# Kernel optimization log

Measured on AMD Instinct MI355X. Metric: run time of the kernel, lower is better.

The kernel has to match this reference:

```python
import jax, jax.numpy as jnp
import numpy as np


def setup_inputs() -> dict:
    key = jax.random.key(0)
    k1, k2, k3 = jax.random.split(key, 3)
    N, M, D, K = 8192, 8192, 512, 128
    x = jax.random.normal(k1, (N, D), dtype=jnp.float32)
    target = jax.random.normal(k2, (M, D), dtype=jnp.float32)
    W = jax.random.normal(k3, (D, K), dtype=jnp.float32) * 0.05
    return {"x": x, "target": target, "W": W}


def reference(x, target, W):
    # phi_Brenier(x): convex potential f(x) = logsumexp(x @ W)  -> [N]
    phi_b = jax.nn.logsumexp(x @ W, axis=-1)
    # phi_Kantorovich = 0.5||x||^2 - phi_Brenier  -> [N]
    x_sq = jnp.sum(x * x, axis=-1)
    phi_k = 0.5 * x_sq - phi_b
    t_sq = jnp.sum(target * target, axis=-1)
    DD = 0.5 * (x_sq[:, None] + t_sq[None, :] - 2.0 * (x @ target.T))
    # C-transform: min over source points  -> [M]
    phi_c = jnp.min(DD - phi_k[:, None], axis=0)
    # Kantorovich dual objective (scalar)
    return jnp.mean(phi_k) + jnp.mean(phi_c)
```

## Files before the change

### kernel.cpp

```cpp
#include <hip/hip_runtime.h>
#include <hip/hip_bf16.h>
#include <stdint.h>

typedef __attribute__((ext_vector_type(8))) short short8;
typedef __attribute__((ext_vector_type(4))) float f32x4;
typedef __attribute__((ext_vector_type(16))) float f32x16;
typedef __attribute__((ext_vector_type(4))) int i32x4;
typedef __attribute__((ext_vector_type(8))) int i32x8;

#define N_PTS 8192
#define M_PTS 8192
#define DIM   512
#define KDIM  128

__device__ __forceinline__ unsigned fenc(float f) {
  unsigned u = __float_as_uint(f);
  return (u & 0x80000000u) ? ~u : (u | 0x80000000u);
}
__device__ __forceinline__ float fdec(unsigned k) {
  unsigned u = (k & 0x80000000u) ? (k ^ 0x80000000u) : ~k;
  return __uint_as_float(u);
}

__device__ __forceinline__ unsigned short f2bf(float f) {
  union { __hip_bfloat16 h; unsigned short u; } c;
  c.h = __float2bfloat16(f);
  return c.u;
}

__device__ __forceinline__ unsigned f2e4m3(float f) {
  unsigned u = __float_as_uint(f);
  unsigned s = (u >> 24) & 0x80;
  unsigned mag = u & 0x7fffffffu;
  unsigned r = mag + 0x0007ffffu + ((mag >> 20) & 1u);
  int e = (int)(r >> 23) - 127;
  if (e < -6) return s;
  unsigned m = (r >> 20) & 7u;
  return s | (unsigned)((e + 7) << 3) | m;
}

__device__ __forceinline__ void async_copy16(const void* g, void* l) {
  __builtin_amdgcn_global_load_lds(
      (const __attribute__((address_space(1))) void*)g,
      (__attribute__((address_space(3))) void*)l, 16, 0, 0);
}

__device__ __forceinline__ int swz_slot(int row, int slot) {
  return slot ^ ((row >> 1) & 3);
}

__device__ __forceinline__ int chunk_key(int row) {
  return ((row >> 1) & 3) ^ ((row >> 3) & 1) ^ (((row >> 4) & 1) << 1);
}

#define BARRIER __builtin_amdgcn_s_barrier()

__global__ __launch_bounds__(256)
void prep_all_kernel(const float* __restrict__ x, const float* __restrict__ tgt,
                     const float* __restrict__ W,
                     unsigned short* __restrict__ Xb, unsigned char* __restrict__ Xf8,
                     unsigned char* __restrict__ TfT, unsigned short* __restrict__ WbT,
                     float* __restrict__ xsq, float* __restrict__ tsq,
                     unsigned* __restrict__ keys) {
  const int bid = blockIdx.x;
  const int tid = threadIdx.x;
  if (bid >= (N_PTS + M_PTS) / 4) {
    const int o = (bid - (N_PTS + M_PTS) / 4) * 256 + tid;
    const int k = o >> 9, d = o & 511;
    WbT[o] = f2bf(W[d * KDIM + k]);
    return;
  }
  const int gw = (bid * 256 + tid) >> 6;
  const int j = tid & 63;
  float s;
  if (gw < N_PTS) {
    const float* src = x + (size_t)gw * DIM + j * 8;
    float4 v0 = *(const float4*)src;
    float4 v1 = *(const float4*)(src + 4);
    s = v0.x * v0.x + v0.y * v0.y + v0.z * v0.z + v0.w * v0.w +
        v1.x * v1.x + v1.y * v1.y + v1.z * v1.z + v1.w * v1.w;
    unsigned short* db = Xb + (size_t)gw * DIM + j * 8;
    ushort4 ob0, ob1;
    ob0.x = f2bf(v0.x); ob0.y = f2bf(v0.y); ob0.z = f2bf(v0.z); ob0.w = f2bf(v0.w);
    ob1.x = f2bf(v1.x); ob1.y = f2bf(v1.y); ob1.z = f2bf(v1.z); ob1.w = f2bf(v1.w);
    *(ushort4*)db = ob0;
    *(ushort4*)(db + 4) = ob1;
    unsigned long long p = (unsigned long long)f2e4m3(v0.x)
        | ((unsigned long long)f2e4m3(v0.y) << 8)
        | ((unsigned long long)f2e4m3(v0.z) << 16)
        | ((unsigned long long)f2e4m3(v0.w) << 24)
        | ((unsigned long long)f2e4m3(v1.x) << 32)
        | ((unsigned long long)f2e4m3(v1.y) << 40)
        | ((unsigned long long)f2e4m3(v1.z) << 48)
        | ((unsigned long long)f2e4m3(v1.w) << 56);
    *(unsigned long long*)(Xf8 + (size_t)gw * DIM + j * 8) = p;
#pragma unroll
    for (int m = 1; m <= 32; m <<= 1) s += __shfl_xor(s, m);
    if (j == 0) xsq[gw] = s;
  } else {
    const int tr = gw - N_PTS;
    const float* src = tgt + (size_t)tr * DIM + j * 8;
    float4 v0 = *(const float4*)src;
    float4 v1 = *(const float4*)(src + 4);
    s = v0.x * v0.x + v0.y * v0.y + v0.z * v0.z + v0.w * v0.w +
        v1.x * v1.x + v1.y * v1.y + v1.z * v1.z + v1.w * v1.w;
    unsigned long long p = (unsigned long long)f2e4m3(v0.x)
        | ((unsigned long long)f2e4m3(v0.y) << 8)
        | ((unsigned long long)f2e4m3(v0.z) << 16)
        | ((unsigned long long)f2e4m3(v0.w) << 24)
        | ((unsigned long long)f2e4m3(v1.x) << 32)
        | ((unsigned long long)f2e4m3(v1.y) << 40)
        | ((unsigned long long)f2e4m3(v1.z) << 48)
        | ((unsigned long long)f2e4m3(v1.w) << 56);
    *(unsigned long long*)(TfT + ((size_t)(j >> 3) * M_PTS + tr) * 64 + (j & 7) * 8) = p;
#pragma unroll
    for (int m = 1; m <= 32; m <<= 1) s += __shfl_xor(s, m);
    if (j == 0) { tsq[tr] = s; keys[tr] = 0xFFFFFFFFu; }
  }
}

__global__ __launch_bounds__(256)
void phi_b_kernel(const short* __restrict__ Xb, const short* __restrict__ WbT,
                  float* __restrict__ phi_b) {
  __shared__ __align__(16) short As[32 * 32];
  __shared__ __align__(16) short Bs[128 * 32];
  __shared__ __align__(16) float lg[32][136];

  const int tid = threadIdx.x;
  const int wave = tid >> 6, lane = tid & 63;
  const int n0 = blockIdx.x * 32;
  const int fr = lane & 15, g = lane >> 4;
  const int wc = wave;

  const int srow = tid >> 2;
  const int sk8 = swz_slot(srow, tid & 3) * 8;
  const int ra = tid >> 2;
  const int ska = swz_slot(ra, tid & 3) * 8;

  f32x4 acc[2][2] = {};
  for (int kt = 0; kt < 16; ++kt) {
    const int k0 = kt * 32;
    if (wave < 2)
      async_copy16(Xb + (size_t)(n0 + ra) * DIM + k0 + ska, &As[wave * 512]);
    async_copy16(WbT + (size_t)srow * DIM + k0 + sk8, &Bs[wave * 512]);
    async_copy16(WbT + (size_t)(srow + 64) * DIM + k0 + sk8, &Bs[2048 + wave * 512]);
    __syncthreads();
    short8 a[2], b[2];
#pragma unroll
    for (int i = 0; i < 2; ++i) {
      const int R = i * 16 + fr;
      a[i] = *(const short8*)&As[R * 32 + swz_slot(R, g) * 8];
    }
#pragma unroll
    for (int jx = 0; jx < 2; ++jx) {
      const int R = wc * 32 + jx * 16 + fr;
      b[jx] = *(const short8*)&Bs[R * 32 + swz_slot(R, g) * 8];
    }
#pragma unroll
    for (int i = 0; i < 2; ++i)
#pragma unroll
      for (int jx = 0; jx < 2; ++jx)
        acc[i][jx] = __builtin_amdgcn_mfma_f32_16x16x32_bf16(a[i], b[jx], acc[i][jx], 0, 0, 0);
    __syncthreads();
  }

  const int rq = g * 4;
#pragma unroll
  for (int i = 0; i < 2; ++i)
#pragma unroll
    for (int jx = 0; jx < 2; ++jx)
#pragma unroll
      for (int q = 0; q < 4; ++q)
        lg[i * 16 + rq + q][wc * 32 + jx * 16 + fr] = acc[i][jx][q];
  __syncthreads();

  const int row = tid >> 3, c8 = tid & 7;
  const float4* lr = (const float4*)(&lg[row][c8 * 16]);
  float mx = -3.4e38f;
#pragma unroll
  for (int c = 0; c < 4; ++c) {
    float4 v = lr[c];
    mx = fmaxf(mx, fmaxf(fmaxf(v.x, v.y), fmaxf(v.z, v.w)));
  }
  mx = fmaxf(mx, __shfl_xor(mx, 1));
  mx = fmaxf(mx, __shfl_xor(mx, 2));
  mx = fmaxf(mx, __shfl_xor(mx, 4));
  float s = 0.f;
#pragma unroll
  for (int c = 0; c < 4; ++c) {
    float4 v = lr[c];
    s += __expf(v.x - mx) + __expf(v.y - mx) + __expf(v.z - mx) + __expf(v.w - mx);
  }
  s += __shfl_xor(s, 1);
  s += __shfl_xor(s, 2);
  s += __shfl_xor(s, 4);
  if (c8 == 0) phi_b[n0 + row] = mx + logf(s);
}

__device__ __forceinline__ void stgA(const unsigned char* __restrict__ mat,
                                     int rowbase, int kbyte,
                                     unsigned char* dst, int tid) {
  const int r = tid >> 2, d = tid & 3;
  async_copy16(mat + (size_t)(rowbase + r) * DIM + kbyte + ((d ^ chunk_key(r)) << 4),
               dst + (tid >> 6) * 1024);
}

__device__ __forceinline__ i32x8 ld2x16(const unsigned char* p0, const unsigned char* p1) {
  i32x4 lo = *(const i32x4*)p0;
  i32x4 hi = *(const i32x4*)p1;
  return __builtin_shufflevector(lo, hi, 0, 1, 2, 3, 4, 5, 6, 7);
}

__device__ __forceinline__ f32x16 mfma_mx(i32x8 a, i32x8 b, f32x16 c) {
  return __builtin_amdgcn_mfma_scale_f32_32x32x64_f8f6f4(a, b, c, 0, 0,
                                                         0, 0x7F, 0, 0x7F);
}

template <int VMC, bool STG, bool LDB, bool BAR>
__device__ __forceinline__ void ktile(const unsigned char* Abuf, unsigned char* Sbuf,
                                      const unsigned char* __restrict__ Xf,
                                      const unsigned char* __restrict__ Bnx,
                                      int n0, int kstage, int tid, int aoff,
                                      i32x8 (&fb)[2], i32x8 (&fbn)[2],
                                      f32x16 (&acc)[4][2]) {
  i32x8 fa[4];
#pragma unroll
  for (int i = 0; i < 4; ++i)
    fa[i] = ld2x16(Abuf + aoff + i * 2048, Abuf + ((aoff + i * 2048) ^ 16));
  if (LDB) {
    fbn[0] = ld2x16(Bnx, Bnx + 16);
    fbn[1] = ld2x16(Bnx + 2048, Bnx + 2048 + 16);
  }
  if (STG) {
    stgA(Xf, n0, kstage, Sbuf, tid);
    stgA(Xf, n0 + 128, kstage, Sbuf + 8192, tid);
  }
  __builtin_amdgcn_s_setprio(1);
#pragma unroll
  for (int i = 0; i < 4; ++i) acc[i][0] = mfma_mx(fa[i], fb[0], acc[i][0]);
#pragma unroll
  for (int i = 0; i < 4; ++i) acc[i][1] = mfma_mx(fa[i], fb[1], acc[i][1]);
  __builtin_amdgcn_s_setprio(0);
  if (VMC == 6) asm volatile("s_waitcnt vmcnt(6)" ::: "memory");
  else if (VMC == 4) asm volatile("s_waitcnt vmcnt(4)" ::: "memory");
  else if (VMC == 0) asm volatile("s_waitcnt vmcnt(0)" ::: "memory");
  if (BAR) BARRIER;
}

__global__ __launch_bounds__(512, 2)
void gemm_min_kernel(const unsigned char* __restrict__ Xf, const unsigned char* __restrict__ TfT,
                     const float* __restrict__ phi_b, unsigned* __restrict__ keys) {
  __shared__ __align__(16) unsigned char lds8[49152];

  const int tid = threadIdx.x;
  const int wave = tid >> 6, lane = tid & 63;
  const int wm = wave >> 2, wn = wave & 3;
  const int fr5 = lane & 31, h = lane >> 5;

  const int bid = blockIdx.x;
  const int xcd = bid & 7, idx = bid >> 3;
  const int nt = (xcd >> 1) * 8 + (idx >> 4);
  const int mt = (xcd & 1) * 16 + (idx & 15);
  const int n0 = nt * 256, m0 = mt * 256;

  const int aoff = (wm * 128 + fr5) * 64 + (((h << 1) ^ chunk_key(fr5)) << 4);

  const unsigned char* Bb = TfT + ((size_t)(m0 + wn * 64 + fr5)) * 64 + h * 32;
#define BK_T(kt) (Bb + (size_t)(kt) * (M_PTS * 64))

  unsigned char* B0 = lds8;
  unsigned char* B1 = lds8 + 16384;
  unsigned char* B2 = lds8 + 32768;

  stgA(Xf, n0, 0, B0, tid);       stgA(Xf, n0 + 128, 0, B0 + 8192, tid);
  stgA(Xf, n0, 64, B1, tid);      stgA(Xf, n0 + 128, 64, B1 + 8192, tid);
  asm volatile("s_waitcnt vmcnt(0)" ::: "memory");
  BARRIER;

  i32x8 s0[2], s1[2], s2[2];
  s0[0] = ld2x16(BK_T(0), BK_T(0) + 16);
  s0[1] = ld2x16(BK_T(0) + 2048, BK_T(0) + 2048 + 16);
  s1[0] = ld2x16(BK_T(1), BK_T(1) + 16);
  s1[1] = ld2x16(BK_T(1) + 2048, BK_T(1) + 2048 + 16);

  f32x16 acc[4][2] = {};
  ktile<6, true, true, true>(B0, B2, Xf, BK_T(2), n0, 128, tid, aoff, s0, s2, acc);
  ktile<6, true, true, true>(B1, B0, Xf, BK_T(3), n0, 192, tid, aoff, s1, s0, acc);
  ktile<6, true, true, true>(B2, B1, Xf, BK_T(4), n0, 256, tid, aoff, s2, s1, acc);
  ktile<6, true, true, true>(B0, B2, Xf, BK_T(5), n0, 320, tid, aoff, s0, s2, acc);
  ktile<6, true, true, true>(B1, B0, Xf, BK_T(6), n0, 384, tid, aoff, s1, s0, acc);
  ktile<6, true, true, true>(B2, B1, Xf, BK_T(7), n0, 448, tid, aoff, s2, s1, acc);
  ktile<0, false, false, true>(B0, B2, Xf, BK_T(7), n0, 0, tid, aoff, s0, s2, acc);
  ktile<-1, false, false, false>(B1, B2, Xf, BK_T(7), n0, 0, tid, aoff, s1, s2, acc);

  float mv0 = 3.4e38f, mv1 = 3.4e38f;
#pragma unroll
  for (int i = 0; i < 4; ++i) {
    float pb[16];
#pragma unroll
    for (int q = 0; q < 16; ++q)
      pb[q] = phi_b[n0 + wm * 128 + i * 32 + (q & 3) + 8 * (q >> 2) + 4 * h];
#pragma unroll
    for (int q = 0; q < 16; ++q) {
      mv0 = fminf(mv0, pb[q] - acc[i][0][q]);
      mv1 = fminf(mv1, pb[q] - acc[i][1][q]);
    }
  }
  mv0 = fminf(mv0, __shfl_xor(mv0, 32));
  mv1 = fminf(mv1, __shfl_xor(mv1, 32));
  if (h == 0) {
    atomicMin(&keys[m0 + wn * 64 + fr5], fenc(mv0));
    atomicMin(&keys[m0 + wn * 64 + 32 + fr5], fenc(mv1));
  }
#undef BK_T
}

__global__ __launch_bounds__(256)
void partial_kernel(const float* __restrict__ xsq, const float* __restrict__ phi_b,
                    const float* __restrict__ tsq, const unsigned* __restrict__ keys,
                    double* __restrict__ partials) {
  const int b = blockIdx.x, t = threadIdx.x;
  double s;
  if (b < 32) {
    const int n = b * 256 + t;
    s = 0.5 * (double)xsq[n] - (double)phi_b[n];
  } else {
    const int m = (b - 32) * 256 + t;
    s = 0.5 * (double)tsq[m] + (double)fdec(keys[m]);
  }
  const int lane = t & 63, wv = t >> 6;
#pragma unroll
  for (int k = 1; k <= 32; k <<= 1) s += __shfl_xor(s, k);
  __shared__ double ps[4];
  if (lane == 0) ps[wv] = s;
  __syncthreads();
  if (t == 0) partials[b] = ps[0] + ps[1] + ps[2] + ps[3];
}

__global__ __launch_bounds__(64)
void final_kernel(const double* __restrict__ partials, float* __restrict__ out) {
  if (threadIdx.x == 0) {
    double a = 0.0, c = 0.0;
#pragma unroll
    for (int i = 0; i < 32; ++i) a += partials[i];
#pragma unroll
    for (int i = 32; i < 64; ++i) c += partials[i];
    out[0] = (float)(a / N_PTS + c / M_PTS);
  }
}

extern "C" void kernel_launch(void* const* d_in, const int* in_sizes, int n_in,
                              void* d_out, int out_size, void* d_ws, size_t ws_size,
                              hipStream_t stream) {
  const float* x = (const float*)d_in[0];
  const float* tgt = (const float*)d_in[1];
  const float* W = (const float*)d_in[2];

  char* ws = (char*)d_ws;
  const size_t XB_BYTES = (size_t)N_PTS * DIM * 2;
  const size_t XF_BYTES = (size_t)N_PTS * DIM;
  const size_t TF_BYTES = (size_t)M_PTS * DIM;
  const size_t WT_BYTES = (size_t)KDIM * DIM * 2;
  unsigned short* Xb = (unsigned short*)ws;
  unsigned char* Xf8 = (unsigned char*)(ws + XB_BYTES);
  unsigned char* TfT = (unsigned char*)(ws + XB_BYTES + XF_BYTES);
  unsigned short* WbT = (unsigned short*)(ws + XB_BYTES + XF_BYTES + TF_BYTES);
  float* phi_b = (float*)(ws + XB_BYTES + XF_BYTES + TF_BYTES + WT_BYTES);
  float* xsq = phi_b + N_PTS;
  float* tsq = xsq + N_PTS;
  unsigned* keys = (unsigned*)(tsq + M_PTS);
  double* partials = (double*)(keys + M_PTS + 64);

  const int prep_blocks = (N_PTS + M_PTS) / 4 + (KDIM * DIM) / 256;
  prep_all_kernel<<<prep_blocks, 256, 0, stream>>>(x, tgt, W, Xb, Xf8, TfT, WbT,
                                                   xsq, tsq, keys);
  phi_b_kernel<<<N_PTS / 32, 256, 0, stream>>>((const short*)Xb, (const short*)WbT, phi_b);
  gemm_min_kernel<<<(N_PTS / 256) * (M_PTS / 256), 512, 0, stream>>>(Xf8, TfT, phi_b, keys);
  partial_kernel<<<64, 256, 0, stream>>>(xsq, phi_b, tsq, keys, partials);
  final_kernel<<<1, 64, 0, stream>>>(partials, (float*)d_out);
}
```

Baseline: 65.39 us.

## Stage entire A tile into LDS upfront and drop per-tile barriers

Replaces the triple-buffered A-tile pipeline with a single up-front load of all eight K-stages of the X tile into 128KB of LDS, followed by barrier-free MFMA tiles. This removes the per-iteration vmcnt waits and block barriers. In exchange, launch bounds drop to one block per CU and the global-load latency is no longer overlapped with compute, which lowers occupancy and exposes the full load time.

```diff
diff --git a/kernel.cpp b/kernel.cpp
--- a/kernel.cpp
+++ b/kernel.cpp
@@ -216,13 +216,11 @@
                                                          0, 0x7F, 0, 0x7F);
 }
 
-template <int VMC, bool STG, bool LDB, bool BAR>
-__device__ __forceinline__ void ktile(const unsigned char* Abuf, unsigned char* Sbuf,
-                                      const unsigned char* __restrict__ Xf,
-                                      const unsigned char* __restrict__ Bnx,
-                                      int n0, int kstage, int tid, int aoff,
-                                      i32x8 (&fb)[2], i32x8 (&fbn)[2],
-                                      f32x16 (&acc)[4][2]) {
+template <bool LDB>
+__device__ __forceinline__ void tile_nf(const unsigned char* __restrict__ Abuf,
+                                        const unsigned char* __restrict__ Bnx,
+                                        int aoff, i32x8 (&fb)[2], i32x8 (&fbn)[2],
+                                        f32x16 (&acc)[4][2]) {
   i32x8 fa[4];
 #pragma unroll
   for (int i = 0; i < 4; ++i)
@@ -231,26 +229,18 @@
     fbn[0] = ld2x16(Bnx, Bnx + 16);
     fbn[1] = ld2x16(Bnx + 2048, Bnx + 2048 + 16);
   }
-  if (STG) {
-    stgA(Xf, n0, kstage, Sbuf, tid);
-    stgA(Xf, n0 + 128, kstage, Sbuf + 8192, tid);
-  }
   __builtin_amdgcn_s_setprio(1);
 #pragma unroll
   for (int i = 0; i < 4; ++i) acc[i][0] = mfma_mx(fa[i], fb[0], acc[i][0]);
 #pragma unroll
   for (int i = 0; i < 4; ++i) acc[i][1] = mfma_mx(fa[i], fb[1], acc[i][1]);
   __builtin_amdgcn_s_setprio(0);
-  if (VMC == 6) asm volatile("s_waitcnt vmcnt(6)" ::: "memory");
-  else if (VMC == 4) asm volatile("s_waitcnt vmcnt(4)" ::: "memory");
-  else if (VMC == 0) asm volatile("s_waitcnt vmcnt(0)" ::: "memory");
-  if (BAR) BARRIER;
-}
-
-__global__ __launch_bounds__(512, 2)
+}
+
+__global__ __launch_bounds__(512, 1)
 void gemm_min_kernel(const unsigned char* __restrict__ Xf, const unsigned char* __restrict__ TfT,
                      const float* __restrict__ phi_b, unsigned* __restrict__ keys) {
-  __shared__ __align__(16) unsigned char lds8[49152];
+  __shared__ __align__(16) unsigned char lds8[131072];
 
   const int tid = threadIdx.x;
   const int wave = tid >> 6, lane = tid & 63;
@@ -268,12 +258,11 @@
   const unsigned char* Bb = TfT + ((size_t)(m0 + wn * 64 + fr5)) * 64 + h * 32;
 #define BK_T(kt) (Bb + (size_t)(kt) * (M_PTS * 64))
 
-  unsigned char* B0 = lds8;
-  unsigned char* B1 = lds8 + 16384;
-  unsigned char* B2 = lds8 + 32768;
-
-  stgA(Xf, n0, 0, B0, tid);       stgA(Xf, n0 + 128, 0, B0 + 8192, tid);
-  stgA(Xf, n0, 64, B1, tid);      stgA(Xf, n0 + 128, 64, B1 + 8192, tid);
+#pragma unroll
+  for (int kt = 0; kt < 8; ++kt) {
+    stgA(Xf, n0, kt * 64, lds8 + kt * 16384, tid);
+    stgA(Xf, n0 + 128, kt * 64, lds8 + kt * 16384 + 8192, tid);
+  }
   asm volatile("s_waitcnt vmcnt(0)" ::: "memory");
   BARRIER;
 
@@ -284,14 +273,14 @@
   s1[1] = ld2x16(BK_T(1) + 2048, BK_T(1) + 2048 + 16);
 
   f32x16 acc[4][2] = {};
-  ktile<6, true, true, true>(B0, B2, Xf, BK_T(2), n0, 128, tid, aoff, s0, s2, acc);
-  ktile<6, true, true, true>(B1, B0, Xf, BK_T(3), n0, 192, tid, aoff, s1, s0, acc);
-  ktile<6, true, true, true>(B2, B1, Xf, BK_T(4), n0, 256, tid, aoff, s2, s1, acc);
-  ktile<6, true, true, true>(B0, B2, Xf, BK_T(5), n0, 320, tid, aoff, s0, s2, acc);
-  ktile<6, true, true, true>(B1, B0, Xf, BK_T(6), n0, 384, tid, aoff, s1, s0, acc);
-  ktile<6, true, true, true>(B2, B1, Xf, BK_T(7), n0, 448, tid, aoff, s2, s1, acc);
-  ktile<0, false, false, true>(B0, B2, Xf, BK_T(7), n0, 0, tid, aoff, s0, s2, acc);
-  ktile<-1, false, false, false>(B1, B2, Xf, BK_T(7), n0, 0, tid, aoff, s1, s2, acc);
+  tile_nf<true>(lds8 + 0 * 16384, BK_T(2), aoff, s0, s2, acc);
+  tile_nf<true>(lds8 + 1 * 16384, BK_T(3), aoff, s1, s0, acc);
+  tile_nf<true>(lds8 + 2 * 16384, BK_T(4), aoff, s2, s1, acc);
+  tile_nf<true>(lds8 + 3 * 16384, BK_T(5), aoff, s0, s2, acc);
+  tile_nf<true>(lds8 + 4 * 16384, BK_T(6), aoff, s1, s0, acc);
+  tile_nf<true>(lds8 + 5 * 16384, BK_T(7), aoff, s2, s1, acc);
+  tile_nf<false>(lds8 + 6 * 16384, BK_T(7), aoff, s0, s2, acc);
+  tile_nf<false>(lds8 + 7 * 16384, BK_T(7), aoff, s1, s2, acc);
 
   float mv0 = 3.4e38f, mv1 = 3.4e38f;
 #pragma unroll
```

Result: slower. 67.71 us (+3.5%).
